# Kernel optimization log

Measured on AMD Instinct MI355X. Metric: run time of the kernel, lower is better.

## Reference

```python
import jax, jax.numpy as jnp
import numpy as np

N_NODES = 50000
N_EDGES = 800000
IN_DIM = 256
HID = 32
HEADS = 8
N_CLASSES = 40
NEG_SLOPE = 0.2  # DGL GATConv default


def setup_inputs() -> dict:
    key = jax.random.key(0)
    ks = jax.random.split(key, 9)
    x = jax.random.normal(ks[0], (N_NODES, IN_DIM), dtype=jnp.float32)
    src = jax.random.randint(ks[1], (N_EDGES,), 0, N_NODES)
    dst = jax.random.randint(ks[2], (N_EDGES,), 0, N_NODES)
    s = 0.05
    W1 = jax.random.normal(ks[3], (IN_DIM, HEADS * HID), dtype=jnp.float32) * s
    al1 = jax.random.normal(ks[4], (HEADS, HID), dtype=jnp.float32) * s
    ar1 = jax.random.normal(ks[5], (HEADS, HID), dtype=jnp.float32) * s
    W2 = jax.random.normal(ks[6], (HEADS * HID, N_CLASSES), dtype=jnp.float32) * s
    al2 = jax.random.normal(ks[7], (1, N_CLASSES), dtype=jnp.float32) * s
    ar2 = jax.random.normal(ks[8], (1, N_CLASSES), dtype=jnp.float32) * s
    return {"x": x, "src": src, "dst": dst, "W1": W1, "al1": al1, "ar1": ar1,
            "W2": W2, "al2": al2, "ar2": ar2}


def gat_conv(h, src, dst, W, al, ar, heads, dout):
    # h: [N, F_in]; W: [F_in, heads*dout]; al/ar: [heads, dout]
    feat = (h @ W).reshape(-1, heads, dout)               # [N, H, D]
    el = (feat * al).sum(-1)                               # [N, H]
    er = (feat * ar).sum(-1)                               # [N, H]
    e = jax.nn.leaky_relu(el[src] + er[dst], NEG_SLOPE)    # [E, H]
    # segment softmax over incoming edges of each dst node
    emax = jax.ops.segment_max(e, dst, num_segments=N_NODES)
    emax = lax_stop(jnp.where(jnp.isfinite(emax), emax, 0.0))
    ee = jnp.exp(e - emax[dst])                            # [E, H]
    denom = jax.ops.segment_sum(ee, dst, num_segments=N_NODES)
    alpha = ee / denom[dst]                                # [E, H]
    msg = feat[src] * alpha[:, :, None]                    # [E, H, D]
    return jax.ops.segment_sum(msg, dst, num_segments=N_NODES)  # [N, H, D]


def lax_stop(v):
    return jax.lax.stop_gradient(v)


def reference(x, src, dst, W1, al1, ar1, W2, al2, ar2):
    # eval mode: feat dropout is identity
    h = gat_conv(x, src, dst, W1, al1, ar1, HEADS, HID)    # [N, 8, 32]
    h = jax.nn.relu(h.reshape(N_NODES, HEADS * HID))       # flatten(1) + relu
    h = gat_conv(h, src, dst, W2, al2, ar2, 1, N_CLASSES)  # [N, 1, C]
    h = h.mean(axis=1)                                     # [N, C]
    return jax.nn.log_softmax(h, axis=1)
```

## Files before the change

### kernel.cpp

```cpp
#include <hip/hip_runtime.h>
#include <hip/hip_bf16.h>
#include <math.h>

#define N_NODES 50000
#define N_EDGES 800000
#define IN_DIM  256
#define HID     32
#define HEADS   8
#define NCLS    40
#define NEG     0.2f
#define CAP1    128
#define CAP2    128

using short8  = __attribute__((ext_vector_type(8))) short;
using f32x4   = __attribute__((ext_vector_type(4))) float;
using floatx2 = __attribute__((ext_vector_type(2))) float;

__device__ __forceinline__ float leaky(float x) { return x >= 0.f ? x : NEG * x; }
__device__ __forceinline__ unsigned short f2b(float f) {
    unsigned int u = __float_as_uint(f);
    unsigned int r = (u + 0x7fffu + ((u >> 16) & 1u)) >> 16;
    return (unsigned short)r;
}
__device__ __forceinline__ float b2f(unsigned short h) {
    return __uint_as_float((unsigned int)h << 16);
}


__global__ void cvt_hist_k(const float* __restrict__ W1, const float* __restrict__ W2,
                           unsigned short* __restrict__ BTile, unsigned short* __restrict__ W2T,
                           const int* __restrict__ dst, int* __restrict__ deg,
                           int* __restrict__ rank) {
    if (blockIdx.x < 256) {
        int n = blockIdx.x, k = threadIdx.x;
        BTile[(size_t)(k >> 5) * 8192 + n * 32 + (k & 31)] = f2b(W1[k * 256 + n]);
        if (n < 48) {
            int half = k >> 7, cs = (k & 127) >> 3, ni = k & 7;
            int ck = half * 128 + ni * 16 + cs;
            W2T[n * 256 + k] = (n < 40) ? f2b(W2[ck * 40 + n]) : (unsigned short)0;
        }
    } else {
        int e4 = (blockIdx.x - 256) * 256 + threadIdx.x;
        if (e4 * 4 >= N_EDGES) return;
        int4 d = *reinterpret_cast<const int4*>(dst + e4 * 4);
        int4 rk;
        rk.x = atomicAdd(&deg[d.x], 1);
        rk.y = atomicAdd(&deg[d.y], 1);
        rk.z = atomicAdd(&deg[d.z], 1);
        rk.w = atomicAdd(&deg[d.w], 1);
        *reinterpret_cast<int4*>(rank + e4 * 4) = rk;
    }
}

__global__ __launch_bounds__(256) void gemm1_scatter_k(const float* __restrict__ A,
                                                       const unsigned short* __restrict__ BTile,
                                                       unsigned char* __restrict__ F8, int M,
                                                       int gblocks,
                                                       const int* __restrict__ src,
                                                       const int* __restrict__ dst,
                                                       const int* __restrict__ rank,
                                                       const int* __restrict__ offs,
                                                       int* __restrict__ ssorted) {
    __shared__ unsigned short Asm[2][64][40];
    __shared__ unsigned short Bsm[2][256][40];
    if (blockIdx.x >= gblocks) {
        int e4 = (blockIdx.x - gblocks) * 256 + threadIdx.x;
        if (e4 * 4 >= N_EDGES) return;
        int4 d  = *reinterpret_cast<const int4*>(dst + e4 * 4);
        int4 sv = *reinterpret_cast<const int4*>(src + e4 * 4);
        int4 rk = *reinterpret_cast<const int4*>(rank + e4 * 4);
        ssorted[offs[d.x] + rk.x] = sv.x;
        ssorted[offs[d.y] + rk.y] = sv.y;
        ssorted[offs[d.z] + rk.z] = sv.z;
        ssorted[offs[d.w] + rk.w] = sv.w;
        return;
    }
    int t = threadIdx.x;
    int lane = t & 63, w = t >> 6;
    int wr = w >> 1, wc = w & 1;
    int m0 = blockIdx.x * 64;
    int rsub = lane & 15, koff = (lane >> 4) * 8;
    f32x4 acc[2][8] = {};

    int ar = t >> 2, ac = (t & 3) * 8;
    const float* ap = A + (size_t)(m0 + ar) * 256 + ac;
    bool aok = (m0 + ar) < M;
    const unsigned short* bp = BTile + (size_t)t * 32;

    float4 a0 = make_float4(0.f, 0.f, 0.f, 0.f), a1 = a0;
    if (aok) { a0 = *reinterpret_cast<const float4*>(ap); a1 = *reinterpret_cast<const float4*>(ap + 4); }
    uint4 b0 = *reinterpret_cast<const uint4*>(bp);
    uint4 b1 = *reinterpret_cast<const uint4*>(bp + 8);
    uint4 b2 = *reinterpret_cast<const uint4*>(bp + 16);
    uint4 b3 = *reinterpret_cast<const uint4*>(bp + 24);
    {
        short8 bb;
        bb[0] = (short)f2b(a0.x); bb[1] = (short)f2b(a0.y); bb[2] = (short)f2b(a0.z); bb[3] = (short)f2b(a0.w);
        bb[4] = (short)f2b(a1.x); bb[5] = (short)f2b(a1.y); bb[6] = (short)f2b(a1.z); bb[7] = (short)f2b(a1.w);
        *reinterpret_cast<short8*>(&Asm[0][ar][ac]) = bb;
        *reinterpret_cast<uint4*>(&Bsm[0][t][0])  = b0;
        *reinterpret_cast<uint4*>(&Bsm[0][t][8])  = b1;
        *reinterpret_cast<uint4*>(&Bsm[0][t][16]) = b2;
        *reinterpret_cast<uint4*>(&Bsm[0][t][24]) = b3;
    }
    __syncthreads();

    for (int kt = 0; kt < 8; ++kt) {
        if (kt < 7) {
            a0 = make_float4(0.f, 0.f, 0.f, 0.f); a1 = a0;
            if (aok) {
                const float* p = ap + (kt + 1) * 32;
                a0 = *reinterpret_cast<const float4*>(p);
                a1 = *reinterpret_cast<const float4*>(p + 4);
            }
            const unsigned short* nb = bp + (size_t)(kt + 1) * 8192;
            b0 = *reinterpret_cast<const uint4*>(nb);
            b1 = *reinterpret_cast<const uint4*>(nb + 8);
            b2 = *reinterpret_cast<const uint4*>(nb + 16);
            b3 = *reinterpret_cast<const uint4*>(nb + 24);
        }
        short8 a[2], b[8];
#pragma unroll
        for (int mi = 0; mi < 2; mi++)
            a[mi] = *reinterpret_cast<const short8*>(&Asm[kt & 1][wr * 32 + mi * 16 + rsub][koff]);
#pragma unroll
        for (int ni = 0; ni < 8; ni++)
            b[ni] = *reinterpret_cast<const short8*>(&Bsm[kt & 1][wc * 128 + ni * 16 + rsub][koff]);
#pragma unroll
        for (int mi = 0; mi < 2; mi++)
#pragma unroll
            for (int ni = 0; ni < 8; ni++)
                acc[mi][ni] = __builtin_amdgcn_mfma_f32_16x16x32_bf16(a[mi], b[ni], acc[mi][ni], 0, 0, 0);
        if (kt < 7) {
            int nb2 = (kt + 1) & 1;
            short8 bb;
            bb[0] = (short)f2b(a0.x); bb[1] = (short)f2b(a0.y); bb[2] = (short)f2b(a0.z); bb[3] = (short)f2b(a0.w);
            bb[4] = (short)f2b(a1.x); bb[5] = (short)f2b(a1.y); bb[6] = (short)f2b(a1.z); bb[7] = (short)f2b(a1.w);
            *reinterpret_cast<short8*>(&Asm[nb2][ar][ac]) = bb;
            *reinterpret_cast<uint4*>(&Bsm[nb2][t][0])  = b0;
            *reinterpret_cast<uint4*>(&Bsm[nb2][t][8])  = b1;
            *reinterpret_cast<uint4*>(&Bsm[nb2][t][16]) = b2;
            *reinterpret_cast<uint4*>(&Bsm[nb2][t][24]) = b3;
            __syncthreads();
        }
    }

    int rgrp = (lane >> 4) * 4, csub = lane & 15;
#pragma unroll
    for (int mi = 0; mi < 2; mi++) {
#pragma unroll
        for (int i = 0; i < 4; i++) {
            int r = m0 + wr * 32 + mi * 16 + rgrp + i;
            if (r < M) {
                int d0 = __builtin_amdgcn_cvt_pk_fp8_f32(acc[mi][0][i], acc[mi][1][i], 0, false);
                d0 = __builtin_amdgcn_cvt_pk_fp8_f32(acc[mi][2][i], acc[mi][3][i], d0, true);
                int d1 = __builtin_amdgcn_cvt_pk_fp8_f32(acc[mi][4][i], acc[mi][5][i], 0, false);
                d1 = __builtin_amdgcn_cvt_pk_fp8_f32(acc[mi][6][i], acc[mi][7][i], d1, true);
                uint2 st; st.x = (unsigned)d0; st.y = (unsigned)d1;
                *reinterpret_cast<uint2*>(F8 + (size_t)r * 256 + wc * 128 + csub * 8) = st;
            }
        }
    }
}

__global__ __launch_bounds__(256) void elr1_k(const unsigned char* __restrict__ feat8,
                                              const float* __restrict__ al,
                                              const float* __restrict__ ar,
                                              float* __restrict__ el, float* __restrict__ er) {
    int wid = (blockIdx.x * blockDim.x + threadIdx.x) >> 6;
    int lane = threadIdx.x & 63;
    if (wid >= N_NODES) return;
    unsigned u = *reinterpret_cast<const unsigned*>(feat8 + (size_t)wid * 256 + 4 * lane);
    floatx2 lo = __builtin_amdgcn_cvt_pk_f32_fp8((int)u, false);
    floatx2 hi = __builtin_amdgcn_cvt_pk_f32_fp8((int)u, true);
    int csub = (lane & 31) >> 1;
    int h0 = (lane >> 5) * 4 + 2 * (lane & 1);
    float pl0 = lo.x * al[h0 * 32 + csub] + lo.y * al[h0 * 32 + 16 + csub];
    float pr0 = lo.x * ar[h0 * 32 + csub] + lo.y * ar[h0 * 32 + 16 + csub];
    float pl1 = hi.x * al[(h0 + 1) * 32 + csub] + hi.y * al[(h0 + 1) * 32 + 16 + csub];
    float pr1 = hi.x * ar[(h0 + 1) * 32 + csub] + hi.y * ar[(h0 + 1) * 32 + 16 + csub];
#pragma unroll
    for (int d = 2; d <= 16; d <<= 1) {
        pl0 += __shfl_xor(pl0, d); pr0 += __shfl_xor(pr0, d);
        pl1 += __shfl_xor(pl1, d); pr1 += __shfl_xor(pr1, d);
    }
    if (csub == 0) {
        el[wid * 8 + h0] = pl0; el[wid * 8 + h0 + 1] = pl1;
        er[wid * 8 + h0] = pr0; er[wid * 8 + h0 + 1] = pr1;
    }
}

__global__ __launch_bounds__(256) void gemm2_mfma(const unsigned short* __restrict__ A,
                                                  const unsigned short* __restrict__ BT,
                                                  const float* __restrict__ al2,
                                                  const float* __restrict__ ar2,
                                                  unsigned short* __restrict__ C,
                                                  float* __restrict__ el2,
                                                  float* __restrict__ er2, int M) {
    __shared__ unsigned short Asm[2][64][40];
    int t = threadIdx.x;
    int lane = t & 63, w = t >> 6;
    int m0 = blockIdx.x * 64;
    int rsub = lane & 15, koff = (lane >> 4) * 8;
    f32x4 acc[3] = {};

    int r_t = t >> 2, c8 = (t & 3) * 8;
    const unsigned short* ap = A + (size_t)(m0 + r_t) * 256 + c8;
    bool arow_ok = (m0 + r_t) < M;

    uint4 s0 = make_uint4(0, 0, 0, 0);
    if (arow_ok) s0 = *reinterpret_cast<const uint4*>(ap);
    *reinterpret_cast<uint4*>(&Asm[0][r_t][c8]) = s0;
    __syncthreads();

    for (int kt = 0; kt < 8; ++kt) {
        if (kt < 7) {
            s0 = make_uint4(0, 0, 0, 0);
            if (arow_ok) s0 = *reinterpret_cast<const uint4*>(ap + (kt + 1) * 32);
        }
        short8 b[3], a;
#pragma unroll
        for (int ni = 0; ni < 3; ni++)
            b[ni] = *reinterpret_cast<const short8*>(BT + (size_t)(ni * 16 + rsub) * 256 + kt * 32 + koff);
        a = *reinterpret_cast<const short8*>(&Asm[kt & 1][w * 16 + rsub][koff]);
#pragma unroll
        for (int ni = 0; ni < 3; ni++)
            acc[ni] = __builtin_amdgcn_mfma_f32_16x16x32_bf16(a, b[ni], acc[ni], 0, 0, 0);
        if (kt < 7) {
            *reinterpret_cast<uint4*>(&Asm[(kt + 1) & 1][r_t][c8]) = s0;
            __syncthreads();
        }
    }

    int rgrp = (lane >> 4) * 4, csub = lane & 15;
    float alc[3], arc[3];
#pragma unroll
    for (int ni = 0; ni < 3; ni++) {
        int col = ni * 16 + csub;
        alc[ni] = (col < 40) ? al2[col] : 0.f;
        arc[ni] = (col < 40) ? ar2[col] : 0.f;
    }
#pragma unroll
    for (int i = 0; i < 4; i++) {
        int r = m0 + w * 16 + rgrp + i;
        float pl = acc[0][i] * alc[0] + acc[1][i] * alc[1] + acc[2][i] * alc[2];
        float pr = acc[0][i] * arc[0] + acc[1][i] * arc[1] + acc[2][i] * arc[2];
        pl += __shfl_xor(pl, 1); pl += __shfl_xor(pl, 2);
        pl += __shfl_xor(pl, 4); pl += __shfl_xor(pl, 8);
        pr += __shfl_xor(pr, 1); pr += __shfl_xor(pr, 2);
        pr += __shfl_xor(pr, 4); pr += __shfl_xor(pr, 8);
        if (r < M) {
#pragma unroll
            for (int ni = 0; ni < 3; ni++) {
                int col = ni * 16 + csub;
                if (col < 40) C[(size_t)r * 40 + col] = f2b(acc[ni][i]);
            }
            if (csub == 0) { el2[r] = pl; er2[r] = pr; }
        }
    }
}

__global__ void scan1_k(const int* __restrict__ deg, int* __restrict__ offs,
                        int* __restrict__ bsum, int n) {
    __shared__ int s[256];
    int tid = threadIdx.x;
    int i = blockIdx.x * 256 + tid;
    int v = (i < n) ? deg[i] : 0;
    s[tid] = v;
    __syncthreads();
    for (int d = 1; d < 256; d <<= 1) {
        int t = (tid >= d) ? s[tid - d] : 0;
        __syncthreads();
        s[tid] += t;
        __syncthreads();
    }
    if (i < n) offs[i] = s[tid] - v;
    if (tid == 255) bsum[blockIdx.x] = s[255];
}

__global__ void scan3_k(int* __restrict__ offs, const int* __restrict__ bsum,
                        int n, int nb) {
    __shared__ int red[256];
    int tid = threadIdx.x;
    int v = (tid < blockIdx.x && tid < nb) ? bsum[tid] : 0;
    red[tid] = v;
    __syncthreads();
#pragma unroll
    for (int d = 128; d > 0; d >>= 1) {
        if (tid < d) red[tid] += red[tid + d];
        __syncthreads();
    }
    int prefix = red[0];
    int i = blockIdx.x * 256 + tid;
    if (i < n) offs[i] += prefix;
    if (i == 0) offs[n] = N_EDGES;
}

__global__ __launch_bounds__(256) void agg1_k(const unsigned char* __restrict__ feat8,
                                              const float* __restrict__ el,
                                              const float* __restrict__ er,
                                              const int* __restrict__ offs,
                                              const int* __restrict__ ssorted,
                                              unsigned short* __restrict__ h1) {
    __shared__ float sa[4][CAP1 * 8];
    __shared__ int   ss[4][CAP1];
    int t = threadIdx.x;
    int wv = t >> 6, lane = t & 63;
    int n = blockIdx.x * 4 + wv;
    if (n >= N_NODES) return;
    int beg = offs[n];
    int deg = offs[n + 1] - beg;
    int eloc = lane >> 3, h = lane & 7;
    int h0 = (lane >> 5) * 4 + 2 * (lane & 1);
    float er_h = er[n * 8 + h];

    float acc0 = 0.f, acc1 = 0.f, acc2 = 0.f, acc3 = 0.f;

    if (deg <= CAP1) {
        float ssum = 0.f;
        int c0 = 0;
        for (; c0 + 32 <= deg; c0 += 32) {
#pragma unroll
            for (int q = 0; q < 4; q++) {
                int idx = c0 + q * 8 + eloc;
                int s = ssorted[beg + idx];
                if (h == 0) ss[wv][idx] = s;
                float ee = __expf(leaky(el[s * 8 + h] + er_h));
                sa[wv][idx * 8 + h] = ee;
                ssum += ee;
            }
        }
        for (; c0 < deg; c0 += 8) {
            int idx = c0 + eloc;
            if (idx < deg) {
                int s = ssorted[beg + idx];
                if (h == 0) ss[wv][idx] = s;
                float ee = __expf(leaky(el[s * 8 + h] + er_h));
                sa[wv][idx * 8 + h] = ee;
                ssum += ee;
            }
        }
        ssum += __shfl_xor(ssum, 8);
        ssum += __shfl_xor(ssum, 16);
        ssum += __shfl_xor(ssum, 32);
        float inv = 1.f / ssum;
        float iv0 = __shfl(inv, h0), iv1 = __shfl(inv, h0 + 1);
        asm volatile("s_waitcnt lgkmcnt(0)" ::: "memory");
        for (c0 = 0; c0 < deg; c0 += 32) {
            int nr = deg - c0; if (nr > 32) nr = 32;
            unsigned u[32];
#pragma unroll
            for (int j = 0; j < 32; j++) {
                if (j < nr) {
                    int sj = ss[wv][c0 + j];
                    u[j] = *reinterpret_cast<const unsigned*>(feat8 + (size_t)sj * 256 + 4 * lane);
                }
            }
#pragma unroll
            for (int j = 0; j < 32; j++) {
                if (j < nr) {
                    float2 av = *reinterpret_cast<const float2*>(&sa[wv][(c0 + j) * 8 + h0]);
                    floatx2 lo = __builtin_amdgcn_cvt_pk_f32_fp8((int)u[j], false);
                    floatx2 hi = __builtin_amdgcn_cvt_pk_f32_fp8((int)u[j], true);
                    acc0 += av.x * lo.x;
                    acc1 += av.x * lo.y;
                    acc2 += av.y * hi.x;
                    acc3 += av.y * hi.y;
                }
            }
        }
        acc0 *= iv0; acc1 *= iv0; acc2 *= iv1; acc3 *= iv1;
    } else {
        float ssum = 0.f;
        for (int c0 = 0; c0 < deg; c0 += 8) {
            bool act = (c0 + eloc) < deg;
            float ee = 0.f;
            if (act) {
                int s = ssorted[beg + c0 + eloc];
                ee = __expf(leaky(el[s * 8 + h] + er_h));
            }
            ssum += ee;
        }
        ssum += __shfl_xor(ssum, 8);
        ssum += __shfl_xor(ssum, 16);
        ssum += __shfl_xor(ssum, 32);
        float inv = 1.f / ssum;
        float iv0 = __shfl(inv, h0), iv1 = __shfl(inv, h0 + 1);
        for (int c0 = 0; c0 < deg; c0 += 8) {
            int nr = deg - c0; if (nr > 8) nr = 8;
            int s = 0; float a = 0.f;
            if (eloc < nr) {
                s = ssorted[beg + c0 + eloc];
                a = __expf(leaky(el[s * 8 + h] + er_h));
            }
#pragma unroll
            for (int j = 0; j < 8; j++) {
                if (j < nr) {
                    int   sj = __shfl(s, j * 8);
                    float a0 = __shfl(a, j * 8 + h0) * iv0;
                    float a1 = __shfl(a, j * 8 + h0 + 1) * iv1;
                    unsigned u = *reinterpret_cast<const unsigned*>(feat8 + (size_t)sj * 256 + 4 * lane);
                    floatx2 lo = __builtin_amdgcn_cvt_pk_f32_fp8((int)u, false);
                    floatx2 hi = __builtin_amdgcn_cvt_pk_f32_fp8((int)u, true);
                    acc0 += a0 * lo.x;
                    acc1 += a0 * lo.y;
                    acc2 += a1 * hi.x;
                    acc3 += a1 * hi.y;
                }
            }
        }
    }
    ushort4 o;
    o.x = f2b(fmaxf(acc0, 0.f));
    o.y = f2b(fmaxf(acc1, 0.f));
    o.z = f2b(fmaxf(acc2, 0.f));
    o.w = f2b(fmaxf(acc3, 0.f));
    *reinterpret_cast<ushort4*>(h1 + (size_t)n * 256 + 4 * lane) = o;
}

__global__ __launch_bounds__(256) void agg2_k(const unsigned short* __restrict__ feat2q,
                                              const float* __restrict__ el2,
                                              const float* __restrict__ er2,
                                              const int* __restrict__ offs,
                                              const int* __restrict__ ssorted,
                                              float* __restrict__ out) {
    __shared__ float sa[4][CAP2];
    __shared__ int   ss[4][CAP2];
    int t = threadIdx.x;
    int wv = t >> 6, lane = t & 63;
    int n = blockIdx.x * 4 + wv;
    if (n >= N_NODES) return;
    int beg = offs[n];
    int deg = offs[n + 1] - beg;
    float ern = er2[n];
    int eloc = lane >> 3, c8 = lane & 7;

    float acc[8] = {};
    if (deg <= CAP2) {
        float ssum = 0.f;
        for (int c0 = 0; c0 < deg; c0 += 64) {
            int idx = c0 + lane;
            if (idx < deg) {
                int s = ssorted[beg + idx];
                ss[wv][idx] = s;
                float ee = __expf(leaky(el2[s] + ern));
                sa[wv][idx] = ee;
                ssum += ee;
            }
        }
#pragma unroll
        for (int d = 1; d < 64; d <<= 1) ssum += __shfl_xor(ssum, d);
        float inv = 1.f / ssum;
        asm volatile("s_waitcnt lgkmcnt(0)" ::: "memory");
        for (int c0 = 0; c0 < deg; c0 += 32) {
            uint4 v[4]; float wgt[4];
#pragma unroll
            for (int q = 0; q < 4; q++) {
                int idx = c0 + q * 8 + eloc;
                v[q] = make_uint4(0, 0, 0, 0); wgt[q] = 0.f;
                if (c8 < 5 && idx < deg) {
                    int s = ss[wv][idx]; wgt[q] = sa[wv][idx];
                    v[q] = *reinterpret_cast<const uint4*>(feat2q + (size_t)s * 40 + c8 * 8);
                }
            }
#pragma unroll
            for (int q = 0; q < 4; q++) {
                const unsigned short* pv = reinterpret_cast<const unsigned short*>(&v[q]);
#pragma unroll
                for (int i = 0; i < 8; i++) acc[i] += wgt[q] * b2f(pv[i]);
            }
        }
#pragma unroll
        for (int i = 0; i < 8; i++) acc[i] *= inv;
    } else {
        float ssum = 0.f;
        for (int c0 = 0; c0 < deg; c0 += 64) {
            bool act = (c0 + lane) < deg;
            if (act) ssum += __expf(leaky(el2[ssorted[beg + c0 + lane]] + ern));
        }
#pragma unroll
        for (int d = 1; d < 64; d <<= 1) ssum += __shfl_xor(ssum, d);
        float inv = 1.f / ssum;
        for (int c0 = 0; c0 < deg; c0 += 8) {
            int nr = deg - c0; if (nr > 8) nr = 8;
            if (eloc < nr && c8 < 5) {
                int s = ssorted[beg + c0 + eloc];
                float a = __expf(leaky(el2[s] + ern)) * inv;
                uint4 v = *reinterpret_cast<const uint4*>(feat2q + (size_t)s * 40 + c8 * 8);
                const unsigned short* pv = reinterpret_cast<const unsigned short*>(&v);
#pragma unroll
                for (int i = 0; i < 8; i++) acc[i] += a * b2f(pv[i]);
            }
        }
    }
#pragma unroll
    for (int i = 0; i < 8; i++) {
        acc[i] += __shfl_xor(acc[i], 8);
        acc[i] += __shfl_xor(acc[i], 16);
        acc[i] += __shfl_xor(acc[i], 32);
    }
    float lmax = -INFINITY;
    if (c8 < 5) {
#pragma unroll
        for (int i = 0; i < 8; i++) lmax = fmaxf(lmax, acc[i]);
    }
    lmax = fmaxf(lmax, __shfl_xor(lmax, 1));
    lmax = fmaxf(lmax, __shfl_xor(lmax, 2));
    lmax = fmaxf(lmax, __shfl_xor(lmax, 4));
    float lsum = 0.f;
    if (c8 < 5) {
#pragma unroll
        for (int i = 0; i < 8; i++) lsum += __expf(acc[i] - lmax);
    }
    lsum += __shfl_xor(lsum, 1);
    lsum += __shfl_xor(lsum, 2);
    lsum += __shfl_xor(lsum, 4);
    if (eloc == 0 && c8 < 5) {
        float lg = __logf(lsum);
        float* o = out + (size_t)n * 40 + c8 * 8;
#pragma unroll
        for (int i = 0; i < 8; i++) o[i] = acc[i] - lmax - lg;
    }
}

extern "C" void kernel_launch(void* const* d_in, const int* in_sizes, int n_in,
                              void* d_out, int out_size, void* d_ws, size_t ws_size,
                              hipStream_t stream) {
    (void)in_sizes; (void)n_in; (void)out_size; (void)ws_size;
    const float* x   = (const float*)d_in[0];
    const int*   src = (const int*)d_in[1];
    const int*   dst = (const int*)d_in[2];
    const float* W1  = (const float*)d_in[3];
    const float* al1 = (const float*)d_in[4];
    const float* ar1 = (const float*)d_in[5];
    const float* W2  = (const float*)d_in[6];
    const float* al2 = (const float*)d_in[7];
    const float* ar2 = (const float*)d_in[8];
    float* out = (float*)d_out;

    char* ws = (char*)d_ws;
    size_t off = 0;
    auto alloc = [&](size_t bytes) {
        void* p = ws + off;
        off += (bytes + 255) & ~(size_t)255;
        return p;
    };
    unsigned short* w1tile = (unsigned short*)alloc((size_t)8 * 256 * 32 * 2);
    unsigned short* w2t    = (unsigned short*)alloc((size_t)48 * 256 * 2);
    unsigned char*  feat8  = (unsigned char*)alloc((size_t)N_NODES * 256);
    unsigned short* h1p    = (unsigned short*)alloc((size_t)N_NODES * 256 * 2);
    unsigned short* feat2q = (unsigned short*)alloc((size_t)N_NODES * 40 * 2);
    float* el1   = (float*)alloc((size_t)N_NODES * 8 * 4);
    float* er1   = (float*)alloc((size_t)N_NODES * 8 * 4);
    float* el2   = (float*)alloc((size_t)N_NODES * 4);
    float* er2   = (float*)alloc((size_t)N_NODES * 4);
    int* deg     = (int*)alloc((size_t)N_NODES * 4);
    int* offs    = (int*)alloc((size_t)(N_NODES + 1) * 4);
    int* rank    = (int*)alloc((size_t)N_EDGES * 4);
    int* bsum    = (int*)alloc(1024 * 4);
    int* ssorted = (int*)alloc((size_t)N_EDGES * 4);

    hipMemsetAsync(deg, 0, (size_t)N_NODES * 4, stream);

    cvt_hist_k<<<256 + (N_EDGES / 4 + 255) / 256, 256, 0, stream>>>(W1, W2, w1tile, w2t, dst, deg, rank);
    int nb = (N_NODES + 255) / 256;
    scan1_k<<<nb, 256, 0, stream>>>(deg, offs, bsum, N_NODES);
    scan3_k<<<nb, 256, 0, stream>>>(offs, bsum, N_NODES, nb);

    int gblocks = (N_NODES + 63) / 64;
    int sblocks = (N_EDGES / 4 + 255) / 256;
    gemm1_scatter_k<<<gblocks + sblocks, 256, 0, stream>>>(x, w1tile, feat8, N_NODES, gblocks,
                                                           src, dst, rank, offs, ssorted);
    elr1_k<<<(N_NODES * 64 + 255) / 256, 256, 0, stream>>>(feat8, al1, ar1, el1, er1);
    agg1_k<<<(N_NODES + 3) / 4, 256, 0, stream>>>(feat8, el1, er1, offs, ssorted, h1p);

    gemm2_mfma<<<(N_NODES + 63) / 64, 256, 0, stream>>>(h1p, w2t, al2, ar2, feat2q, el2, er2, N_NODES);
    agg2_k<<<(N_NODES + 3) / 4, 256, 0, stream>>>(feat2q, el2, er2, offs, ssorted, out);
}
```

Before: 182.1 us.

## Fold attention vectors into W1 and compute el/er inside GEMM1 via extra MFMA

Precomputes W1·al1 and W1·ar1 as a small bf16 weight tile, then computes the per-head el/er scores inside the first GEMM with an extra MFMA column block, dropping the separate elr1 kernel. This removes one launch and a full re-read of the fp8 feature matrix, and el/er now come from the unquantized accumulator rather than fp8 features. The scatter stores into the sorted-source array also become nontemporal. The risks are slightly more work per GEMM wave on one column half and different rounding in the attention logits.

```diff
diff --git a/kernel.cpp b/kernel.cpp
--- a/kernel.cpp
+++ b/kernel.cpp
@@ -28,7 +28,9 @@
 
 
 __global__ void cvt_hist_k(const float* __restrict__ W1, const float* __restrict__ W2,
+                           const float* __restrict__ al1, const float* __restrict__ ar1,
                            unsigned short* __restrict__ BTile, unsigned short* __restrict__ W2T,
+                           unsigned short* __restrict__ wlr,
                            const int* __restrict__ dst, int* __restrict__ deg,
                            int* __restrict__ rank) {
     if (blockIdx.x < 256) {
@@ -39,8 +41,23 @@
             int ck = half * 128 + ni * 16 + cs;
             W2T[n * 256 + k] = (n < 40) ? f2b(W2[ck * 40 + n]) : (unsigned short)0;
         }
+    } else if (blockIdx.x == 256) {
+        int k = threadIdx.x;
+        const float* wrow = W1 + (size_t)k * 256;
+#pragma unroll
+        for (int h = 0; h < 8; h++) {
+            float vl = 0.f, vr = 0.f;
+#pragma unroll
+            for (int d = 0; d < 32; d++) {
+                float w = wrow[h * 32 + d];
+                vl += w * al1[h * 32 + d];
+                vr += w * ar1[h * 32 + d];
+            }
+            wlr[(size_t)(k >> 5) * 512 + h * 32 + (k & 31)]        = f2b(vl);
+            wlr[(size_t)(k >> 5) * 512 + (8 + h) * 32 + (k & 31)]  = f2b(vr);
+        }
     } else {
-        int e4 = (blockIdx.x - 256) * 256 + threadIdx.x;
+        int e4 = (blockIdx.x - 257) * 256 + threadIdx.x;
         if (e4 * 4 >= N_EDGES) return;
         int4 d = *reinterpret_cast<const int4*>(dst + e4 * 4);
         int4 rk;
@@ -54,7 +71,10 @@
 
 __global__ __launch_bounds__(256) void gemm1_scatter_k(const float* __restrict__ A,
                                                        const unsigned short* __restrict__ BTile,
-                                                       unsigned char* __restrict__ F8, int M,
+                                                       const unsigned short* __restrict__ wlr,
+                                                       unsigned char* __restrict__ F8,
+                                                       float* __restrict__ el,
+                                                       float* __restrict__ er, int M,
                                                        int gblocks,
                                                        const int* __restrict__ src,
                                                        const int* __restrict__ dst,
@@ -69,10 +89,10 @@
         int4 d  = *reinterpret_cast<const int4*>(dst + e4 * 4);
         int4 sv = *reinterpret_cast<const int4*>(src + e4 * 4);
         int4 rk = *reinterpret_cast<const int4*>(rank + e4 * 4);
-        ssorted[offs[d.x] + rk.x] = sv.x;
-        ssorted[offs[d.y] + rk.y] = sv.y;
-        ssorted[offs[d.z] + rk.z] = sv.z;
-        ssorted[offs[d.w] + rk.w] = sv.w;
+        __builtin_nontemporal_store(sv.x, &ssorted[offs[d.x] + rk.x]);
+        __builtin_nontemporal_store(sv.y, &ssorted[offs[d.y] + rk.y]);
+        __builtin_nontemporal_store(sv.z, &ssorted[offs[d.z] + rk.z]);
+        __builtin_nontemporal_store(sv.w, &ssorted[offs[d.w] + rk.w]);
         return;
     }
     int t = threadIdx.x;
@@ -81,6 +101,7 @@
     int m0 = blockIdx.x * 64;
     int rsub = lane & 15, koff = (lane >> 4) * 8;
     f32x4 acc[2][8] = {};
+    f32x4 accx[2] = {};
 
     int ar = t >> 2, ac = (t & 3) * 8;
     const float* ap = A + (size_t)(m0 + ar) * 256 + ac;
@@ -131,6 +152,12 @@
 #pragma unroll
             for (int ni = 0; ni < 8; ni++)
                 acc[mi][ni] = __builtin_amdgcn_mfma_f32_16x16x32_bf16(a[mi], b[ni], acc[mi][ni], 0, 0, 0);
+        if (wc == 0) {
+            short8 bx = *reinterpret_cast<const short8*>(wlr + (size_t)kt * 512 + rsub * 32 + koff);
+#pragma unroll
+            for (int mi = 0; mi < 2; mi++)
+                accx[mi] = __builtin_amdgcn_mfma_f32_16x16x32_bf16(a[mi], bx, accx[mi], 0, 0, 0);
+        }
         if (kt < 7) {
             int nb2 = (kt + 1) & 1;
             short8 bb;
@@ -158,35 +185,13 @@
                 d1 = __builtin_amdgcn_cvt_pk_fp8_f32(acc[mi][6][i], acc[mi][7][i], d1, true);
                 uint2 st; st.x = (unsigned)d0; st.y = (unsigned)d1;
                 *reinterpret_cast<uint2*>(F8 + (size_t)r * 256 + wc * 128 + csub * 8) = st;
-            }
-        }
-    }
-}
-
-__global__ __launch_bounds__(256) void elr1_k(const unsigned char* __restrict__ feat8,
-                                              const float* __restrict__ al,
-                                              const float* __restrict__ ar,
-                                              float* __restrict__ el, float* __restrict__ er) {
-    int wid = (blockIdx.x * blockDim.x + threadIdx.x) >> 6;
-    int lane = threadIdx.x & 63;
-    if (wid >= N_NODES) return;
-    unsigned u = *reinterpret_cast<const unsigned*>(feat8 + (size_t)wid * 256 + 4 * lane);
-    floatx2 lo = __builtin_amdgcn_cvt_pk_f32_fp8((int)u, false);
-    floatx2 hi = __builtin_amdgcn_cvt_pk_f32_fp8((int)u, true);
-    int csub = (lane & 31) >> 1;
-    int h0 = (lane >> 5) * 4 + 2 * (lane & 1);
-    float pl0 = lo.x * al[h0 * 32 + csub] + lo.y * al[h0 * 32 + 16 + csub];
-    float pr0 = lo.x * ar[h0 * 32 + csub] + lo.y * ar[h0 * 32 + 16 + csub];
-    float pl1 = hi.x * al[(h0 + 1) * 32 + csub] + hi.y * al[(h0 + 1) * 32 + 16 + csub];
-    float pr1 = hi.x * ar[(h0 + 1) * 32 + csub] + hi.y * ar[(h0 + 1) * 32 + 16 + csub];
-#pragma unroll
-    for (int d = 2; d <= 16; d <<= 1) {
-        pl0 += __shfl_xor(pl0, d); pr0 += __shfl_xor(pr0, d);
-        pl1 += __shfl_xor(pl1, d); pr1 += __shfl_xor(pr1, d);
-    }
-    if (csub == 0) {
-        el[wid * 8 + h0] = pl0; el[wid * 8 + h0 + 1] = pl1;
-        er[wid * 8 + h0] = pr0; er[wid * 8 + h0 + 1] = pr1;
+                if (wc == 0) {
+                    float v = accx[mi][i];
+                    if (csub < 8) el[r * 8 + csub] = v;
+                    else          er[r * 8 + (csub - 8)] = v;
+                }
+            }
+        }
     }
 }
 
@@ -547,6 +552,7 @@
     };
     unsigned short* w1tile = (unsigned short*)alloc((size_t)8 * 256 * 32 * 2);
     unsigned short* w2t    = (unsigned short*)alloc((size_t)48 * 256 * 2);
+    unsigned short* wlr    = (unsigned short*)alloc((size_t)8 * 16 * 32 * 2);
     unsigned char*  feat8  = (unsigned char*)alloc((size_t)N_NODES * 256);
     unsigned short* h1p    = (unsigned short*)alloc((size_t)N_NODES * 256 * 2);
     unsigned short* feat2q = (unsigned short*)alloc((size_t)N_NODES * 40 * 2);
@@ -562,16 +568,17 @@
 
     hipMemsetAsync(deg, 0, (size_t)N_NODES * 4, stream);
 
-    cvt_hist_k<<<256 + (N_EDGES / 4 + 255) / 256, 256, 0, stream>>>(W1, W2, w1tile, w2t, dst, deg, rank);
+    cvt_hist_k<<<257 + (N_EDGES / 4 + 255) / 256, 256, 0, stream>>>(W1, W2, al1, ar1,
+                                                                    w1tile, w2t, wlr, dst, deg, rank);
     int nb = (N_NODES + 255) / 256;
     scan1_k<<<nb, 256, 0, stream>>>(deg, offs, bsum, N_NODES);
     scan3_k<<<nb, 256, 0, stream>>>(offs, bsum, N_NODES, nb);
 
     int gblocks = (N_NODES + 63) / 64;
     int sblocks = (N_EDGES / 4 + 255) / 256;
-    gemm1_scatter_k<<<gblocks + sblocks, 256, 0, stream>>>(x, w1tile, feat8, N_NODES, gblocks,
+    gemm1_scatter_k<<<gblocks + sblocks, 256, 0, stream>>>(x, w1tile, wlr, feat8, el1, er1,
+                                                           N_NODES, gblocks,
                                                            src, dst, rank, offs, ssorted);
-    elr1_k<<<(N_NODES * 64 + 255) / 256, 256, 0, stream>>>(feat8, al1, ar1, el1, er1);
     agg1_k<<<(N_NODES + 3) / 4, 256, 0, stream>>>(feat8, el1, er1, offs, ssorted, h1p);
 
     gemm2_mfma<<<(N_NODES + 63) / 64, 256, 0, stream>>>(h1p, w2t, al2, ar2, feat2q, el2, er2, N_NODES);
```

Result: no change. 181.1 us (-0.5%).
